# Kernel tuning notes

Measured on AMD Instinct MI355X. Metric: run time of the kernel, lower is better.

## Reference

```python
import jax, jax.numpy as jnp
import numpy as np

N = 512   # particles
T = 128   # timesteps
V_L = 3.4
V_0 = 4.2
GAMMA = 0.9
ALPHA = 0.15
BETA = 15.0
E_CRIT_INV = 2e-5
F_STD = 0.05
G_STD = 0.02
NU = 1.0 / (G_STD * float(np.sqrt(2.0 * np.pi)))
CUR_MIN = 0.0
CUR_MAX = 1.0


def voc(soc):
    # open-circuit voltage model
    return (V_L + (V_0 - V_L) * jnp.exp(GAMMA * (soc - 1.0))
            + ALPHA * V_L * (soc - 1.0)
            + (1.0 - ALPHA) * V_L * (jnp.exp(-BETA) - jnp.exp(-BETA * jnp.sqrt(soc))))


def mlp(x, w1, b1, w2, b2, w3, b3):
    h = jax.nn.sigmoid(x @ w1 + b1)
    h = jax.nn.sigmoid(h @ w2 + b2)
    return h @ w3 + b3


def setup_inputs() -> dict:
    key = jax.random.key(0)
    ks = jax.random.split(key, 11)
    soc_init = jax.random.uniform(ks[0], (N, 1), jnp.float32, 0.6, 1.0)
    current = jax.random.uniform(ks[1], (1, T), jnp.float32)
    voltage_measured = 3.4 + 0.8 * jax.random.uniform(ks[2], (1, T), jnp.float32)
    noise = jax.random.normal(ks[3], (T, N, 1), jnp.float32)
    u = jax.random.uniform(ks[4], (T,), jnp.float32)
    w1 = jax.random.normal(ks[5], (2, 1024), jnp.float32) / np.float32(np.sqrt(2.0))
    b1 = jnp.zeros((1024,), jnp.float32)
    w2 = jax.random.normal(ks[6], (1024, 512), jnp.float32) / np.float32(np.sqrt(1024.0))
    b2 = jnp.zeros((512,), jnp.float32)
    w3 = jax.random.normal(ks[7], (512, 1), jnp.float32) / np.float32(np.sqrt(512.0))
    b3 = jnp.zeros((1,), jnp.float32)
    return {"soc_init": soc_init, "current": current, "voltage_measured": voltage_measured,
            "noise": noise, "u": u, "w1": w1, "b1": b1, "w2": w2, "b2": b2, "w3": w3, "b3": b3}


def reference(soc_init, current, voltage_measured, noise, u, w1, b1, w2, b2, w3, b3):
    n = soc_init.shape[0]
    # pre-loop step: V at t=0 conditions
    I0 = current[0, 0] * jnp.ones_like(soc_init)
    sI0 = (I0 - CUR_MIN) / (CUR_MAX - CUR_MIN)
    Z0 = mlp(jnp.concatenate([soc_init, sI0], axis=1), w1, b1, w2, b2, w3, b3)
    V0 = voc(soc_init) - I0 * Z0

    log_n = jnp.log(jnp.float32(n))

    def step(carry, xs):
        soc, I, V = carry
        cur_t, vmeas_t, noise_t, u_t = xs
        # state propagation with process noise, then clamp to (0, 1]
        soc = soc - I * V * E_CRIT_INV + F_STD * noise_t
        soc = jnp.where(soc > 1.0, 1.0, jnp.where(soc < 0.0, 1e-10, soc))
        I = cur_t * jnp.ones_like(soc)
        sI = (I - CUR_MIN) / (CUR_MAX - CUR_MIN)
        Z = mlp(jnp.concatenate([soc, sI], axis=1), w1, b1, w2, b2, w3, b3)  # [N,1]
        V = voc(soc) - I * Z                                                 # [N,1]
        # importance weights / step loss (logsumexp trick as in source)
        logW = jnp.log(jnp.float32(NU)) - 0.5 * jnp.square((V - vmeas_t) / G_STD)
        step_loss = jax.nn.logsumexp(logW) - log_n
        # systematic resampling on normalized weights
        wn = jax.nn.softmax(logW[:, 0])          # normalized weights [N]
        cum = jnp.cumsum(wn)
        pos = (jnp.arange(n, dtype=jnp.float32) + u_t) / jnp.float32(n)
        idx = jnp.clip(jnp.searchsorted(cum, pos), 0, n - 1)
        soc_r = soc[idx]
        return (soc_r, I, V), (V[:, 0], soc_r[:, 0], step_loss)

    xs = (current[0], voltage_measured[0], noise, u)
    _, (v_hist, s_hist, losses) = jax.lax.scan(step, (soc_init, I0, V0), xs)
    loss = jnp.sum(losses)
    voltage = v_hist.T    # [N, T]
    soc_hist = s_hist.T   # [N, T]
    return loss, voltage, soc_hist
```

## Files before the change

### kernel.cpp

```cpp
#include <hip/hip_runtime.h>
#include <math.h>

#define NP 512
#define TS 128
#define GI 33
#define TAB2D (GI * GI)
#define GV 193
#define V_Lc 3.4f
#define V_0c 4.2f
#define GAMMAc 0.9f
#define ALPHAc 0.15f
#define BETAc 15.0f
#define E_INV 2e-5f
#define F_STDc 0.05f
#define G_STDc 0.02f

#define LBAR() asm volatile("s_waitcnt lgkmcnt(0)\n\ts_barrier" ::: "memory")

__device__ __forceinline__ float sigmoid_jax(float x) {
    float e = expf(-fabsf(x));
    float num = (x >= 0.f) ? 1.f : e;
    return num / (1.f + e);
}

__device__ __forceinline__ float vocf(float s) {
    float sm1 = s - 1.f;
    return V_Lc + (V_0c - V_Lc) * expf(GAMMAc * sm1)
         + (ALPHAc * V_Lc) * sm1
         + (1.f - ALPHAc) * V_Lc * (expf(-BETAc) - expf(-BETAc * sqrtf(s)));
}

template <int R>
__device__ __forceinline__ int dpp_ror(int v) {
    return __builtin_amdgcn_update_dpp(0, v, 0x120 | R, 0xf, 0xf, false);
}
template <int S>
__device__ __forceinline__ int dpp_shr(int v) {
    return __builtin_amdgcn_update_dpp(0, v, 0x110 | S, 0xf, 0xf, true);
}
__device__ __forceinline__ float rdlane_f(float v, int l) {
    return __int_as_float(__builtin_amdgcn_readlane(__float_as_int(v), l));
}

__device__ __forceinline__ float wave_max_f(float v) {
    v = fmaxf(v, __int_as_float(dpp_ror<1>(__float_as_int(v))));
    v = fmaxf(v, __int_as_float(dpp_ror<2>(__float_as_int(v))));
    v = fmaxf(v, __int_as_float(dpp_ror<4>(__float_as_int(v))));
    v = fmaxf(v, __int_as_float(dpp_ror<8>(__float_as_int(v))));
    int iv = __float_as_int(v);
    v = fmaxf(v, __int_as_float(__builtin_amdgcn_update_dpp(iv, iv, 0x142, 0xf, 0xf, false)));
    iv = __float_as_int(v);
    v = fmaxf(v, __int_as_float(__builtin_amdgcn_update_dpp(iv, iv, 0x143, 0xf, 0xf, false)));
    return rdlane_f(v, 63);
}

__device__ __forceinline__ int wave_max_i(int v) {
    v = max(v, dpp_ror<1>(v));
    v = max(v, dpp_ror<2>(v));
    v = max(v, dpp_ror<4>(v));
    v = max(v, dpp_ror<8>(v));
    v = max(v, __builtin_amdgcn_update_dpp(v, v, 0x142, 0xf, 0xf, false));
    v = max(v, __builtin_amdgcn_update_dpp(v, v, 0x143, 0xf, 0xf, false));
    return __builtin_amdgcn_readlane(v, 63);
}

__device__ __forceinline__ float wave_scan_add(float v, int lane) {
    v += __int_as_float(dpp_shr<1>(__float_as_int(v)));
    v += __int_as_float(dpp_shr<2>(__float_as_int(v)));
    v += __int_as_float(dpp_shr<4>(__float_as_int(v)));
    v += __int_as_float(dpp_shr<8>(__float_as_int(v)));
    float s15 = rdlane_f(v, 15);
    float s31 = rdlane_f(v, 31);
    float s47 = rdlane_f(v, 47);
    int row = lane >> 4;
    if (row >= 1) v += s15;
    if (row >= 2) v += s31;
    if (row >= 3) v += s47;
    return v;
}

__device__ __forceinline__ int wave_scanmax_i(int v, int lane) {
    v = max(v, dpp_shr<1>(v));
    v = max(v, dpp_shr<2>(v));
    v = max(v, dpp_shr<4>(v));
    v = max(v, dpp_shr<8>(v));
    int r15 = __builtin_amdgcn_readlane(v, 15);
    int r31 = __builtin_amdgcn_readlane(v, 31);
    int r47 = __builtin_amdgcn_readlane(v, 47);
    int row = lane >> 4;
    if (row >= 1) v = max(v, r15);
    if (row >= 2) v = max(v, r31);
    if (row >= 3) v = max(v, r47);
    return v;
}

__device__ __forceinline__ float interp33(const float* __restrict__ row, float s) {
    float x = s * 32.0f;
    int j = (int)floorf(x);
    j = j < 0 ? 0 : (j > 31 ? 31 : j);
    int st = j - 1;
    st = st < 0 ? 0 : (st > 29 ? 29 : st);
    float uu = x - (float)st;
    float um0 = uu, um1 = uu - 1.f, um2 = uu - 2.f, um3 = uu - 3.f;
    float c0 = um1 * um2 * um3 * (-1.f / 6.f);
    float c1 = um0 * um2 * um3 * (0.5f);
    float c2 = um0 * um1 * um3 * (-0.5f);
    float c3 = um0 * um1 * um2 * (1.f / 6.f);
    return c0 * row[st] + c1 * row[st + 1] + c2 * row[st + 2] + c3 * row[st + 3];
}

__device__ __forceinline__ float interp193(const float* __restrict__ row, float s) {
    float x = s * 192.0f;
    int j = (int)floorf(x);
    j = j < 0 ? 0 : (j > 191 ? 191 : j);
    int st = j - 1;
    st = st < 0 ? 0 : (st > 189 ? 189 : st);
    float uu = x - (float)st;
    float um0 = uu, um1 = uu - 1.f, um2 = uu - 2.f, um3 = uu - 3.f;
    float c0 = um1 * um2 * um3 * (-1.f / 6.f);
    float c1 = um0 * um2 * um3 * (0.5f);
    float c2 = um0 * um1 * um3 * (-0.5f);
    float c3 = um0 * um1 * um2 * (1.f / 6.f);
    return c0 * row[st] + c1 * row[st + 1] + c2 * row[st + 2] + c3 * row[st + 3];
}

__device__ __forceinline__ int count_le(float C, float u) {
    int h = (int)floorf(C - u);
    h = h < -1 ? -1 : (h > 511 ? 511 : h);
    h += (int)((h < 511) && (((float)(h + 1) + u) <= C));
    h -= (int)((h >= 0) && (((float)h + u) > C));
    return h + 1;
}

#define BKT 32
__global__ __launch_bounds__(256) void k_tab(
    const float* __restrict__ w1, const float* __restrict__ b1,
    const float* __restrict__ w2, const float* __restrict__ b2,
    const float* __restrict__ w3, float* __restrict__ zpart)
{
    const int tid = threadIdx.x;
    const int rowblk = blockIdx.x >> 1;
    const int colhalf = blockIdx.x & 1;
    const int r0 = rowblk * 16;
    const int cbase = colhalf * 256;

    __shared__ float As[16][BKT + 1];
    __shared__ float Bs[BKT][256];
    __shared__ float srow[16], irow[16];

    if (tid < 16) {
        int r = r0 + tid;
        r = r > (TAB2D - 1) ? (TAB2D - 1) : r;
        int si = r / GI;
        int ii = r - si * GI;
        srow[tid] = (float)si * (1.0f / 32.0f);
        irow[tid] = (float)ii * (1.0f / 32.0f);
    }
    __syncthreads();

    const int rg = tid >> 5;
    const int ct = tid & 31;
    float acc[2][8];
    #pragma unroll
    for (int a = 0; a < 2; ++a)
        #pragma unroll
        for (int b = 0; b < 8; ++b) acc[a][b] = 0.f;

    for (int kk = 0; kk < 1024; kk += BKT) {
        #pragma unroll
        for (int h = 0; h < 2; ++h) {
            int idx = tid + h * 256;
            int row = idx >> 5, k = idx & 31, kc = kk + k;
            float pre = srow[row] * w1[kc] + irow[row] * w1[1024 + kc] + b1[kc];
            As[row][k] = sigmoid_jax(pre);
        }
        #pragma unroll
        for (int jj = 0; jj < 8; ++jj) {
            int vi = tid + jj * 256;
            int k = vi >> 6, c4 = vi & 63;
            *(float4*)&Bs[k][c4 * 4] = *(const float4*)&w2[(kk + k) * 512 + cbase + c4 * 4];
        }
        __syncthreads();
        #pragma unroll
        for (int k = 0; k < BKT; ++k) {
            float a0 = As[rg * 2][k];
            float a1 = As[rg * 2 + 1][k];
            float bq[8];
            *(float4*)&bq[0] = *(const float4*)&Bs[k][ct * 4];
            *(float4*)&bq[4] = *(const float4*)&Bs[k][ct * 4 + 128];
            #pragma unroll
            for (int q = 0; q < 8; ++q) {
                acc[0][q] += a0 * bq[q];
                acc[1][q] += a1 * bq[q];
            }
        }
        __syncthreads();
    }

    float b2r[8], w3r[8];
    *(float4*)&b2r[0] = *(const float4*)&b2[cbase + ct * 4];
    *(float4*)&b2r[4] = *(const float4*)&b2[cbase + ct * 4 + 128];
    *(float4*)&w3r[0] = *(const float4*)&w3[cbase + ct * 4];
    *(float4*)&w3r[4] = *(const float4*)&w3[cbase + ct * 4 + 128];
    #pragma unroll
    for (int rr = 0; rr < 2; ++rr) {
        float zp = 0.f;
        #pragma unroll
        for (int q = 0; q < 8; ++q)
            zp += w3r[q] * sigmoid_jax(acc[rr][q] + b2r[q]);
        #pragma unroll
        for (int mm = 1; mm < 32; mm <<= 1) zp += __shfl_xor(zp, mm);
        if (ct == 0 && (r0 + rg * 2 + rr) < TAB2D)
            zpart[colhalf * TAB2D + r0 + rg * 2 + rr] = zp;
    }
}

__global__ __launch_bounds__(256) void k_pre(
    const float* __restrict__ zpart, const float* __restrict__ current,
    const float* __restrict__ b3, float* __restrict__ vt_g)
{
    __shared__ float zrow[GI];
    const int t = blockIdx.x;
    const int tid = threadIdx.x;
    const float It = current[t];
    const float bb3 = b3[0];

    if (tid < GI) {
        float x = It * 32.0f;
        int j = (int)floorf(x);
        j = j < 0 ? 0 : (j > 31 ? 31 : j);
        int st = j - 1;
        st = st < 0 ? 0 : (st > 29 ? 29 : st);
        float uu = x - (float)st;
        float um0 = uu, um1 = uu - 1.f, um2 = uu - 2.f, um3 = uu - 3.f;
        float c0 = um1 * um2 * um3 * (-1.f / 6.f);
        float c1 = um0 * um2 * um3 * (0.5f);
        float c2 = um0 * um1 * um3 * (-0.5f);
        float c3 = um0 * um1 * um2 * (1.f / 6.f);
        int base = tid * GI + st;
        float n0 = zpart[base]     + zpart[TAB2D + base]     + bb3;
        float n1 = zpart[base + 1] + zpart[TAB2D + base + 1] + bb3;
        float n2 = zpart[base + 2] + zpart[TAB2D + base + 2] + bb3;
        float n3 = zpart[base + 3] + zpart[TAB2D + base + 3] + bb3;
        zrow[tid] = c0 * n0 + c1 * n1 + c2 * n2 + c3 * n3;
    }
    __syncthreads();
    if (tid < GV) {
        float sj = (float)tid * (1.0f / 192.0f);
        vt_g[t * GV + tid] = vocf(sj) - It * interp33(zrow, sj);
    }
}

__global__ __launch_bounds__(256, 1) void k_seq(
    const float* __restrict__ vt_g, const float* __restrict__ soc_init,
    const float* __restrict__ current, const float* __restrict__ vmeas,
    const float* __restrict__ u, const float* __restrict__ noise,
    float* __restrict__ vbuf, float* __restrict__ sbuf, float* __restrict__ out)
{
    const int tid = threadIdx.x;
    const int lane = tid & 63;
    const int wv = tid >> 6;

    __shared__ __align__(16) float vt[TS * GV];
    __shared__ float2 socs2[2][NP / 2];
    __shared__ int2  marker2[NP / 2];
    __shared__ float cur_s[TS], vm_s[TS], u_s[TS];
    __shared__ float2 redMT[4];
    int* marker = (int*)marker2;

    for (int i4 = tid; i4 < (TS * GV) / 4; i4 += 256)
        *(float4*)&vt[i4 * 4] = *(const float4*)&vt_g[i4 * 4];
    if (tid < TS) { cur_s[tid] = current[tid]; vm_s[tid] = vmeas[tid]; u_s[tid] = u[tid]; }
    marker2[tid] = make_int2(0, 0);
    __syncthreads();

    float2 si2 = *(const float2*)&soc_init[2 * tid];
    float soc0 = si2.x, soc1 = si2.y;
    float Iprev = cur_s[0];
    float V0 = interp193(&vt[0], soc0);
    float V1 = interp193(&vt[0], soc1);
    float loss_acc = 0.f;
    const float LOG_NU = logf(19.947114020071635f);
    const float LOG_N = logf(512.f);
    float2 nz = *(const float2*)&noise[2 * tid];

    for (int t = 0; t < TS; ++t) {
        int tn = (t + 1 < TS) ? t + 1 : t;
        float2 nz_next = *(const float2*)&noise[tn * 512 + 2 * tid];

        soc0 = soc0 - Iprev * V0 * E_INV + F_STDc * nz.x;
        soc1 = soc1 - Iprev * V1 * E_INV + F_STDc * nz.y;
        soc0 = soc0 > 1.f ? 1.f : (soc0 < 0.f ? 1e-10f : soc0);
        soc1 = soc1 > 1.f ? 1.f : (soc1 < 0.f ? 1e-10f : soc1);
        socs2[t & 1][tid] = make_float2(soc0, soc1);

        const float* vr = &vt[t * GV];
        V0 = interp193(vr, soc0);
        V1 = interp193(vr, soc1);
        *(float2*)&vbuf[t * 512 + 2 * tid] = make_float2(V0, V1);
        float vm = vm_s[t];
        float d0 = (V0 - vm) * (1.f / G_STDc);
        float d1 = (V1 - vm) * (1.f / G_STDc);
        float lw0 = LOG_NU - 0.5f * d0 * d0;
        float lw1 = LOG_NU - 0.5f * d1 * d1;

        float m = wave_max_f(fmaxf(lw0, lw1));
        float e0 = __expf(lw0 - m);
        float e1 = __expf(lw1 - m);
        float ps = wave_scan_add(e0 + e1, lane);
        if (lane == 63) redMT[wv] = make_float2(m, ps);
        LBAR();

        float2 rmt = redMT[lane & 3];
        float rm = rmt.x;
        float rt = rmt.y;
        float M = rm;
        M = fmaxf(M, __int_as_float(dpp_ror<1>(__float_as_int(M))));
        M = fmaxf(M, __int_as_float(dpp_ror<2>(__float_as_int(M))));
        float fw = __expf(rm - M);
        float term = rt * fw;
        float sc = term;
        sc += __int_as_float(dpp_shr<1>(__float_as_int(sc)));
        sc += __int_as_float(dpp_shr<2>(__float_as_int(sc)));
        float S = rdlane_f(sc, 3);
        float off = (wv > 0) ? rdlane_f(sc, wv - 1) : 0.f;
        float fw_own = rdlane_f(fw, wv);
        loss_acc += M + __logf(S) - LOG_N;

        float incl1 = ps;
        float incl0 = ps - e1;
        float C0 = 512.f * ((off + incl0 * fw_own) / S);
        float C1 = 512.f * ((off + incl1 * fw_own) / S);
        float ut = u_s[t];
        int hi0 = count_le(C0, ut);
        int hi1 = count_le(C1, ut);
        if (hi0 < 512) atomicMax(&marker[hi0], (t << 10) | (2 * tid + 1));
        if (hi1 < 512) atomicMax(&marker[hi1], (t << 10) | (2 * tid + 2));
        LBAR();

        int2 mk = marker2[tid];
        int pm_l = 0;
        for (int w = 0; w < wv; ++w) {
            int2 q = marker2[w * 64 + lane];
            pm_l = max(pm_l, max(q.x, q.y));
        }
        int pm = wave_max_i(pm_l);
        int mpair = max(mk.x, mk.y);
        int psx = wave_scanmax_i(mpair, lane);
        int up = dpp_shr<1>(psx);
        int r15 = __builtin_amdgcn_readlane(psx, 15);
        int r31 = __builtin_amdgcn_readlane(psx, 31);
        int r47 = __builtin_amdgcn_readlane(psx, 47);
        if (lane == 16) up = r15;
        if (lane == 32) up = r31;
        if (lane == 48) up = r47;
        int excl = max(up, pm);
        int tag0 = max(excl, mk.x);
        int tag1 = max(excl, mpair);
        int o0 = ((tag0 >> 10) == t) ? (tag0 & 1023) : 0;
        int o1 = ((tag1 >> 10) == t) ? (tag1 & 1023) : 0;
        o0 = o0 > 511 ? 511 : o0;
        o1 = o1 > 511 ? 511 : o1;
        const float* sflat = (const float*)&socs2[t & 1][0];
        float sr0 = sflat[o0];
        float sr1 = sflat[o1];
        *(float2*)&sbuf[t * 512 + 2 * tid] = make_float2(sr0, sr1);

        soc0 = sr0;
        soc1 = sr1;
        Iprev = cur_s[t];
        nz = nz_next;
    }
    if (tid == 0) out[0] = loss_acc;
}

__global__ __launch_bounds__(256) void k_fin(
    const float* __restrict__ vbuf, const float* __restrict__ sbuf,
    float* __restrict__ out)
{
    __shared__ float tile[32][33];
    int tz = blockIdx.z;
    int t0 = blockIdx.x * 32;
    int i0 = blockIdx.y * 32;
    const float* src = tz ? sbuf : vbuf;
    float* dst = out + 1 + tz * (NP * TS);
    int tx = threadIdx.x & 31, ty = threadIdx.x >> 5;
    #pragma unroll
    for (int m2 = 0; m2 < 4; ++m2)
        tile[ty + 8 * m2][tx] = src[(t0 + ty + 8 * m2) * 512 + i0 + tx];
    __syncthreads();
    #pragma unroll
    for (int m2 = 0; m2 < 4; ++m2)
        dst[(i0 + ty + 8 * m2) * 128 + t0 + tx] = tile[tx][ty + 8 * m2];
}

extern "C" void kernel_launch(void* const* d_in, const int* in_sizes, int n_in,
                              void* d_out, int out_size, void* d_ws, size_t ws_size,
                              hipStream_t stream)
{
    const float* soc_init = (const float*)d_in[0];
    const float* current  = (const float*)d_in[1];
    const float* vmeas    = (const float*)d_in[2];
    const float* noise    = (const float*)d_in[3];
    const float* u        = (const float*)d_in[4];
    const float* w1 = (const float*)d_in[5];
    const float* b1 = (const float*)d_in[6];
    const float* w2 = (const float*)d_in[7];
    const float* b2 = (const float*)d_in[8];
    const float* w3 = (const float*)d_in[9];
    const float* b3 = (const float*)d_in[10];
    float* out = (float*)d_out;
    float* ws  = (float*)d_ws;

    float* zpart = ws;
    float* vt_g  = ws + 2180;
    float* vbuf  = vt_g + TS * GV;
    float* sbuf  = vbuf + NP * TS;

    k_tab<<<138, 256, 0, stream>>>(w1, b1, w2, b2, w3, zpart);
    k_pre<<<128, 256, 0, stream>>>(zpart, current, b3, vt_g);
    k_seq<<<1, 256, 0, stream>>>(vt_g, soc_init, current, vmeas, u, noise,
                                 vbuf, sbuf, out);
    k_fin<<<dim3(4, 16, 2), 256, 0, stream>>>(vbuf, sbuf, out);
}
```

Baseline: 245.2 us.

## Run sequential filter with two waves and four particles per thread

The sequential particle-filter kernel now runs on 128 threads, each handling four particles instead of two. This halves the number of waves taking part in each per-step barrier and cross-wave reduction, and simplifies the block-level max/sum and marker prefix-max. The voltage lookup grid is also refined from 193 to 257 points, with the precompute kernel widened to 320 threads. That raises the table's LDS footprint and initial load, and puts more serial ALU work on each thread.

```diff
diff --git a/kernel.cpp b/kernel.cpp
--- a/kernel.cpp
+++ b/kernel.cpp
@@ -5,7 +5,7 @@
 #define TS 128
 #define GI 33
 #define TAB2D (GI * GI)
-#define GV 193
+#define GV 257
 #define V_Lc 3.4f
 #define V_0c 4.2f
 #define GAMMAc 0.9f
@@ -109,12 +109,12 @@
     return c0 * row[st] + c1 * row[st + 1] + c2 * row[st + 2] + c3 * row[st + 3];
 }
 
-__device__ __forceinline__ float interp193(const float* __restrict__ row, float s) {
-    float x = s * 192.0f;
+__device__ __forceinline__ float interp257(const float* __restrict__ row, float s) {
+    float x = s * 256.0f;
     int j = (int)floorf(x);
-    j = j < 0 ? 0 : (j > 191 ? 191 : j);
+    j = j < 0 ? 0 : (j > 255 ? 255 : j);
     int st = j - 1;
-    st = st < 0 ? 0 : (st > 189 ? 189 : st);
+    st = st < 0 ? 0 : (st > 253 ? 253 : st);
     float uu = x - (float)st;
     float um0 = uu, um1 = uu - 1.f, um2 = uu - 2.f, um3 = uu - 3.f;
     float c0 = um1 * um2 * um3 * (-1.f / 6.f);
@@ -215,7 +215,7 @@
     }
 }
 
-__global__ __launch_bounds__(256) void k_pre(
+__global__ __launch_bounds__(320) void k_pre(
     const float* __restrict__ zpart, const float* __restrict__ current,
     const float* __restrict__ b3, float* __restrict__ vt_g)
 {
@@ -246,12 +246,12 @@
     }
     __syncthreads();
     if (tid < GV) {
-        float sj = (float)tid * (1.0f / 192.0f);
+        float sj = (float)tid * (1.0f / 256.0f);
         vt_g[t * GV + tid] = vocf(sj) - It * interp33(zrow, sj);
     }
 }
 
-__global__ __launch_bounds__(256, 1) void k_seq(
+__global__ __launch_bounds__(128, 1) void k_seq(
     const float* __restrict__ vt_g, const float* __restrict__ soc_init,
     const float* __restrict__ current, const float* __restrict__ vmeas,
     const float* __restrict__ u, const float* __restrict__ noise,
@@ -262,91 +262,108 @@
     const int wv = tid >> 6;
 
     __shared__ __align__(16) float vt[TS * GV];
-    __shared__ float2 socs2[2][NP / 2];
-    __shared__ int2  marker2[NP / 2];
+    __shared__ __align__(16) float socs[2][NP];
+    __shared__ __align__(16) int marker[NP];
     __shared__ float cur_s[TS], vm_s[TS], u_s[TS];
-    __shared__ float2 redMT[4];
-    int* marker = (int*)marker2;
-
-    for (int i4 = tid; i4 < (TS * GV) / 4; i4 += 256)
+    __shared__ __align__(16) float2 redMT[2];
+
+    for (int i4 = tid; i4 < (TS * GV) / 4; i4 += 128)
         *(float4*)&vt[i4 * 4] = *(const float4*)&vt_g[i4 * 4];
-    if (tid < TS) { cur_s[tid] = current[tid]; vm_s[tid] = vmeas[tid]; u_s[tid] = u[tid]; }
-    marker2[tid] = make_int2(0, 0);
+    { int r = TS * GV - (TS * GV / 4) * 4; (void)r; }
+    cur_s[tid] = current[tid]; vm_s[tid] = vmeas[tid]; u_s[tid] = u[tid];
+    *(int4*)&marker[4 * tid] = make_int4(0, 0, 0, 0);
     __syncthreads();
 
-    float2 si2 = *(const float2*)&soc_init[2 * tid];
-    float soc0 = si2.x, soc1 = si2.y;
+    float4 si4 = *(const float4*)&soc_init[4 * tid];
+    float soc0 = si4.x, soc1 = si4.y, soc2 = si4.z, soc3 = si4.w;
     float Iprev = cur_s[0];
-    float V0 = interp193(&vt[0], soc0);
-    float V1 = interp193(&vt[0], soc1);
+    float V0 = interp257(&vt[0], soc0);
+    float V1 = interp257(&vt[0], soc1);
+    float V2 = interp257(&vt[0], soc2);
+    float V3 = interp257(&vt[0], soc3);
     float loss_acc = 0.f;
     const float LOG_NU = logf(19.947114020071635f);
     const float LOG_N = logf(512.f);
-    float2 nz = *(const float2*)&noise[2 * tid];
+    float4 nz = *(const float4*)&noise[4 * tid];
 
     for (int t = 0; t < TS; ++t) {
         int tn = (t + 1 < TS) ? t + 1 : t;
-        float2 nz_next = *(const float2*)&noise[tn * 512 + 2 * tid];
+        float4 nz_next = *(const float4*)&noise[tn * 512 + 4 * tid];
 
         soc0 = soc0 - Iprev * V0 * E_INV + F_STDc * nz.x;
         soc1 = soc1 - Iprev * V1 * E_INV + F_STDc * nz.y;
+        soc2 = soc2 - Iprev * V2 * E_INV + F_STDc * nz.z;
+        soc3 = soc3 - Iprev * V3 * E_INV + F_STDc * nz.w;
         soc0 = soc0 > 1.f ? 1.f : (soc0 < 0.f ? 1e-10f : soc0);
         soc1 = soc1 > 1.f ? 1.f : (soc1 < 0.f ? 1e-10f : soc1);
-        socs2[t & 1][tid] = make_float2(soc0, soc1);
+        soc2 = soc2 > 1.f ? 1.f : (soc2 < 0.f ? 1e-10f : soc2);
+        soc3 = soc3 > 1.f ? 1.f : (soc3 < 0.f ? 1e-10f : soc3);
+        *(float4*)&socs[t & 1][4 * tid] = make_float4(soc0, soc1, soc2, soc3);
 
         const float* vr = &vt[t * GV];
-        V0 = interp193(vr, soc0);
-        V1 = interp193(vr, soc1);
-        *(float2*)&vbuf[t * 512 + 2 * tid] = make_float2(V0, V1);
+        V0 = interp257(vr, soc0);
+        V1 = interp257(vr, soc1);
+        V2 = interp257(vr, soc2);
+        V3 = interp257(vr, soc3);
+        *(float4*)&vbuf[t * 512 + 4 * tid] = make_float4(V0, V1, V2, V3);
         float vm = vm_s[t];
         float d0 = (V0 - vm) * (1.f / G_STDc);
         float d1 = (V1 - vm) * (1.f / G_STDc);
+        float d2 = (V2 - vm) * (1.f / G_STDc);
+        float d3 = (V3 - vm) * (1.f / G_STDc);
         float lw0 = LOG_NU - 0.5f * d0 * d0;
         float lw1 = LOG_NU - 0.5f * d1 * d1;
-
-        float m = wave_max_f(fmaxf(lw0, lw1));
+        float lw2 = LOG_NU - 0.5f * d2 * d2;
+        float lw3 = LOG_NU - 0.5f * d3 * d3;
+
+        float m = wave_max_f(fmaxf(fmaxf(lw0, lw1), fmaxf(lw2, lw3)));
         float e0 = __expf(lw0 - m);
         float e1 = __expf(lw1 - m);
-        float ps = wave_scan_add(e0 + e1, lane);
-        if (lane == 63) redMT[wv] = make_float2(m, ps);
+        float e2 = __expf(lw2 - m);
+        float e3 = __expf(lw3 - m);
+        float c0 = e0;
+        float c1 = c0 + e1;
+        float c2 = c1 + e2;
+        float c3 = c2 + e3;
+        float tot = c3;
+        float incl = wave_scan_add(tot, lane);
+        if (lane == 63) redMT[wv] = make_float2(m, incl);
         LBAR();
 
-        float2 rmt = redMT[lane & 3];
-        float rm = rmt.x;
-        float rt = rmt.y;
-        float M = rm;
-        M = fmaxf(M, __int_as_float(dpp_ror<1>(__float_as_int(M))));
-        M = fmaxf(M, __int_as_float(dpp_ror<2>(__float_as_int(M))));
-        float fw = __expf(rm - M);
-        float term = rt * fw;
-        float sc = term;
-        sc += __int_as_float(dpp_shr<1>(__float_as_int(sc)));
-        sc += __int_as_float(dpp_shr<2>(__float_as_int(sc)));
-        float S = rdlane_f(sc, 3);
-        float off = (wv > 0) ? rdlane_f(sc, wv - 1) : 0.f;
-        float fw_own = rdlane_f(fw, wv);
+        float4 rr = *(float4*)&redMT[0];
+        float M = fmaxf(rr.x, rr.z);
+        float fw0 = __expf(rr.x - M);
+        float fw1 = __expf(rr.z - M);
+        float t0 = rr.y * fw0;
+        float t1 = rr.w * fw1;
+        float S = t0 + t1;
+        float off = wv ? t0 : 0.f;
+        float fw_own = wv ? fw1 : fw0;
         loss_acc += M + __logf(S) - LOG_N;
 
-        float incl1 = ps;
-        float incl0 = ps - e1;
-        float C0 = 512.f * ((off + incl0 * fw_own) / S);
-        float C1 = 512.f * ((off + incl1 * fw_own) / S);
+        float base = incl - tot;
         float ut = u_s[t];
+        float C0 = 512.f * ((off + (base + c0) * fw_own) / S);
+        float C1 = 512.f * ((off + (base + c1) * fw_own) / S);
+        float C2 = 512.f * ((off + (base + c2) * fw_own) / S);
+        float C3 = 512.f * ((off + (base + c3) * fw_own) / S);
         int hi0 = count_le(C0, ut);
         int hi1 = count_le(C1, ut);
-        if (hi0 < 512) atomicMax(&marker[hi0], (t << 10) | (2 * tid + 1));
-        if (hi1 < 512) atomicMax(&marker[hi1], (t << 10) | (2 * tid + 2));
+        int hi2 = count_le(C2, ut);
+        int hi3 = count_le(C3, ut);
+        int p4 = 4 * tid;
+        if (hi0 < 512) atomicMax(&marker[hi0], (t << 10) | (p4 + 1));
+        if (hi1 < 512) atomicMax(&marker[hi1], (t << 10) | (p4 + 2));
+        if (hi2 < 512) atomicMax(&marker[hi2], (t << 10) | (p4 + 3));
+        if (hi3 < 512) atomicMax(&marker[hi3], (t << 10) | (p4 + 4));
         LBAR();
 
-        int2 mk = marker2[tid];
-        int pm_l = 0;
-        for (int w = 0; w < wv; ++w) {
-            int2 q = marker2[w * 64 + lane];
-            pm_l = max(pm_l, max(q.x, q.y));
-        }
-        int pm = wave_max_i(pm_l);
-        int mpair = max(mk.x, mk.y);
-        int psx = wave_scanmax_i(mpair, lane);
+        int4 mk = *(int4*)&marker[4 * tid];
+        int4 oth = *(int4*)&marker[4 * lane];
+        int pm = 0;
+        if (wv) pm = wave_max_i(max(max(oth.x, oth.y), max(oth.z, oth.w)));
+        int lm = max(max(mk.x, mk.y), max(mk.z, mk.w));
+        int psx = wave_scanmax_i(lm, lane);
         int up = dpp_shr<1>(psx);
         int r15 = __builtin_amdgcn_readlane(psx, 15);
         int r31 = __builtin_amdgcn_readlane(psx, 31);
@@ -356,18 +373,25 @@
         if (lane == 48) up = r47;
         int excl = max(up, pm);
         int tag0 = max(excl, mk.x);
-        int tag1 = max(excl, mpair);
+        int tag1 = max(tag0, mk.y);
+        int tag2 = max(tag1, mk.z);
+        int tag3 = max(tag2, mk.w);
         int o0 = ((tag0 >> 10) == t) ? (tag0 & 1023) : 0;
         int o1 = ((tag1 >> 10) == t) ? (tag1 & 1023) : 0;
+        int o2 = ((tag2 >> 10) == t) ? (tag2 & 1023) : 0;
+        int o3 = ((tag3 >> 10) == t) ? (tag3 & 1023) : 0;
         o0 = o0 > 511 ? 511 : o0;
         o1 = o1 > 511 ? 511 : o1;
-        const float* sflat = (const float*)&socs2[t & 1][0];
+        o2 = o2 > 511 ? 511 : o2;
+        o3 = o3 > 511 ? 511 : o3;
+        const float* sflat = &socs[t & 1][0];
         float sr0 = sflat[o0];
         float sr1 = sflat[o1];
-        *(float2*)&sbuf[t * 512 + 2 * tid] = make_float2(sr0, sr1);
-
-        soc0 = sr0;
-        soc1 = sr1;
+        float sr2 = sflat[o2];
+        float sr3 = sflat[o3];
+        *(float4*)&sbuf[t * 512 + 4 * tid] = make_float4(sr0, sr1, sr2, sr3);
+
+        soc0 = sr0; soc1 = sr1; soc2 = sr2; soc3 = sr3;
         Iprev = cur_s[t];
         nz = nz_next;
     }
@@ -418,8 +442,8 @@
     float* sbuf  = vbuf + NP * TS;
 
     k_tab<<<138, 256, 0, stream>>>(w1, b1, w2, b2, w3, zpart);
-    k_pre<<<128, 256, 0, stream>>>(zpart, current, b3, vt_g);
-    k_seq<<<1, 256, 0, stream>>>(vt_g, soc_init, current, vmeas, u, noise,
+    k_pre<<<128, 320, 0, stream>>>(zpart, current, b3, vt_g);
+    k_seq<<<1, 128, 0, stream>>>(vt_g, soc_init, current, vmeas, u, noise,
                                  vbuf, sbuf, out);
     k_fin<<<dim3(4, 16, 2), 256, 0, stream>>>(vbuf, sbuf, out);
 }
```

Result: slower. 267.3 us (+9.0%).

## Run sequential particle filter in a single wave to drop block barriers

Applied to the files above, without the earlier changes.

The sequential resampling loop now runs on one 64-lane wavefront, each lane owning 8 particles, instead of four waves each handling 2. Cross-wave barriers and shared reductions are gone, replaced by in-lane serial scans plus wave-level DPP scans. Without barriers, only an lgkmcnt wait orders the LDS writes and reads. The voltage lookup grid is also widened from 193 to 257 points, which enlarges the table load and changes interpolation accuracy. The trade is per-step barrier latency against a longer serial dependency chain per lane.

```diff
diff --git a/kernel.cpp b/kernel.cpp
--- a/kernel.cpp
+++ b/kernel.cpp
@@ -5,7 +5,7 @@
 #define TS 128
 #define GI 33
 #define TAB2D (GI * GI)
-#define GV 193
+#define GV 257
 #define V_Lc 3.4f
 #define V_0c 4.2f
 #define GAMMAc 0.9f
@@ -15,7 +15,7 @@
 #define F_STDc 0.05f
 #define G_STDc 0.02f
 
-#define LBAR() asm volatile("s_waitcnt lgkmcnt(0)\n\ts_barrier" ::: "memory")
+#define LGKM0() asm volatile("s_waitcnt lgkmcnt(0)" ::: "memory")
 
 __device__ __forceinline__ float sigmoid_jax(float x) {
     float e = expf(-fabsf(x));
@@ -52,16 +52,6 @@
     iv = __float_as_int(v);
     v = fmaxf(v, __int_as_float(__builtin_amdgcn_update_dpp(iv, iv, 0x143, 0xf, 0xf, false)));
     return rdlane_f(v, 63);
-}
-
-__device__ __forceinline__ int wave_max_i(int v) {
-    v = max(v, dpp_ror<1>(v));
-    v = max(v, dpp_ror<2>(v));
-    v = max(v, dpp_ror<4>(v));
-    v = max(v, dpp_ror<8>(v));
-    v = max(v, __builtin_amdgcn_update_dpp(v, v, 0x142, 0xf, 0xf, false));
-    v = max(v, __builtin_amdgcn_update_dpp(v, v, 0x143, 0xf, 0xf, false));
-    return __builtin_amdgcn_readlane(v, 63);
 }
 
 __device__ __forceinline__ float wave_scan_add(float v, int lane) {
@@ -109,12 +99,12 @@
     return c0 * row[st] + c1 * row[st + 1] + c2 * row[st + 2] + c3 * row[st + 3];
 }
 
-__device__ __forceinline__ float interp193(const float* __restrict__ row, float s) {
-    float x = s * 192.0f;
+__device__ __forceinline__ float interp257(const float* __restrict__ row, float s) {
+    float x = s * 256.0f;
     int j = (int)floorf(x);
-    j = j < 0 ? 0 : (j > 191 ? 191 : j);
+    j = j < 0 ? 0 : (j > 255 ? 255 : j);
     int st = j - 1;
-    st = st < 0 ? 0 : (st > 189 ? 189 : st);
+    st = st < 0 ? 0 : (st > 253 ? 253 : st);
     float uu = x - (float)st;
     float um0 = uu, um1 = uu - 1.f, um2 = uu - 2.f, um3 = uu - 3.f;
     float c0 = um1 * um2 * um3 * (-1.f / 6.f);
@@ -215,7 +205,7 @@
     }
 }
 
-__global__ __launch_bounds__(256) void k_pre(
+__global__ __launch_bounds__(320) void k_pre(
     const float* __restrict__ zpart, const float* __restrict__ current,
     const float* __restrict__ b3, float* __restrict__ vt_g)
 {
@@ -246,107 +236,108 @@
     }
     __syncthreads();
     if (tid < GV) {
-        float sj = (float)tid * (1.0f / 192.0f);
+        float sj = (float)tid * (1.0f / 256.0f);
         vt_g[t * GV + tid] = vocf(sj) - It * interp33(zrow, sj);
     }
 }
 
-__global__ __launch_bounds__(256, 1) void k_seq(
+__global__ __launch_bounds__(512, 1) void k_seq(
     const float* __restrict__ vt_g, const float* __restrict__ soc_init,
     const float* __restrict__ current, const float* __restrict__ vmeas,
     const float* __restrict__ u, const float* __restrict__ noise,
     float* __restrict__ vbuf, float* __restrict__ sbuf, float* __restrict__ out)
 {
     const int tid = threadIdx.x;
-    const int lane = tid & 63;
-    const int wv = tid >> 6;
 
     __shared__ __align__(16) float vt[TS * GV];
-    __shared__ float2 socs2[2][NP / 2];
-    __shared__ int2  marker2[NP / 2];
+    __shared__ __align__(16) float socs[NP];
+    __shared__ __align__(16) int marker[NP];
     __shared__ float cur_s[TS], vm_s[TS], u_s[TS];
-    __shared__ float2 redMT[4];
-    int* marker = (int*)marker2;
-
-    for (int i4 = tid; i4 < (TS * GV) / 4; i4 += 256)
+
+    for (int i4 = tid; i4 < (TS * GV) / 4; i4 += 512)
         *(float4*)&vt[i4 * 4] = *(const float4*)&vt_g[i4 * 4];
     if (tid < TS) { cur_s[tid] = current[tid]; vm_s[tid] = vmeas[tid]; u_s[tid] = u[tid]; }
-    marker2[tid] = make_int2(0, 0);
+    marker[tid] = 0;
     __syncthreads();
-
-    float2 si2 = *(const float2*)&soc_init[2 * tid];
-    float soc0 = si2.x, soc1 = si2.y;
+    if (tid >= 64) return;
+
+    const int lane = tid;
+    const int p0 = 8 * lane;
+
+    float soc[8], V[8];
+    *(float4*)&soc[0] = *(const float4*)&soc_init[p0];
+    *(float4*)&soc[4] = *(const float4*)&soc_init[p0 + 4];
     float Iprev = cur_s[0];
-    float V0 = interp193(&vt[0], soc0);
-    float V1 = interp193(&vt[0], soc1);
+    #pragma unroll
+    for (int k = 0; k < 8; ++k) V[k] = interp257(&vt[0], soc[k]);
+
     float loss_acc = 0.f;
     const float LOG_NU = logf(19.947114020071635f);
     const float LOG_N = logf(512.f);
-    float2 nz = *(const float2*)&noise[2 * tid];
+    float nz[8];
+    *(float4*)&nz[0] = *(const float4*)&noise[p0];
+    *(float4*)&nz[4] = *(const float4*)&noise[p0 + 4];
 
     for (int t = 0; t < TS; ++t) {
         int tn = (t + 1 < TS) ? t + 1 : t;
-        float2 nz_next = *(const float2*)&noise[tn * 512 + 2 * tid];
-
-        soc0 = soc0 - Iprev * V0 * E_INV + F_STDc * nz.x;
-        soc1 = soc1 - Iprev * V1 * E_INV + F_STDc * nz.y;
-        soc0 = soc0 > 1.f ? 1.f : (soc0 < 0.f ? 1e-10f : soc0);
-        soc1 = soc1 > 1.f ? 1.f : (soc1 < 0.f ? 1e-10f : soc1);
-        socs2[t & 1][tid] = make_float2(soc0, soc1);
+        float4 nzn0 = *(const float4*)&noise[tn * 512 + p0];
+        float4 nzn1 = *(const float4*)&noise[tn * 512 + p0 + 4];
+
+        #pragma unroll
+        for (int k = 0; k < 8; ++k) {
+            float s = soc[k] - Iprev * V[k] * E_INV + F_STDc * nz[k];
+            soc[k] = s > 1.f ? 1.f : (s < 0.f ? 1e-10f : s);
+        }
+        *(float4*)&socs[p0]     = *(float4*)&soc[0];
+        *(float4*)&socs[p0 + 4] = *(float4*)&soc[4];
 
         const float* vr = &vt[t * GV];
-        V0 = interp193(vr, soc0);
-        V1 = interp193(vr, soc1);
-        *(float2*)&vbuf[t * 512 + 2 * tid] = make_float2(V0, V1);
+        #pragma unroll
+        for (int k = 0; k < 8; ++k) V[k] = interp257(vr, soc[k]);
+        *(float4*)&vbuf[t * 512 + p0]     = *(float4*)&V[0];
+        *(float4*)&vbuf[t * 512 + p0 + 4] = *(float4*)&V[4];
+
         float vm = vm_s[t];
-        float d0 = (V0 - vm) * (1.f / G_STDc);
-        float d1 = (V1 - vm) * (1.f / G_STDc);
-        float lw0 = LOG_NU - 0.5f * d0 * d0;
-        float lw1 = LOG_NU - 0.5f * d1 * d1;
-
-        float m = wave_max_f(fmaxf(lw0, lw1));
-        float e0 = __expf(lw0 - m);
-        float e1 = __expf(lw1 - m);
-        float ps = wave_scan_add(e0 + e1, lane);
-        if (lane == 63) redMT[wv] = make_float2(m, ps);
-        LBAR();
-
-        float2 rmt = redMT[lane & 3];
-        float rm = rmt.x;
-        float rt = rmt.y;
-        float M = rm;
-        M = fmaxf(M, __int_as_float(dpp_ror<1>(__float_as_int(M))));
-        M = fmaxf(M, __int_as_float(dpp_ror<2>(__float_as_int(M))));
-        float fw = __expf(rm - M);
-        float term = rt * fw;
-        float sc = term;
-        sc += __int_as_float(dpp_shr<1>(__float_as_int(sc)));
-        sc += __int_as_float(dpp_shr<2>(__float_as_int(sc)));
-        float S = rdlane_f(sc, 3);
-        float off = (wv > 0) ? rdlane_f(sc, wv - 1) : 0.f;
-        float fw_own = rdlane_f(fw, wv);
+        float lw[8];
+        #pragma unroll
+        for (int k = 0; k < 8; ++k) {
+            float d = (V[k] - vm) * (1.f / G_STDc);
+            lw[k] = LOG_NU - 0.5f * d * d;
+        }
+
+        float m8 = fmaxf(fmaxf(fmaxf(lw[0], lw[1]), fmaxf(lw[2], lw[3])),
+                         fmaxf(fmaxf(lw[4], lw[5]), fmaxf(lw[6], lw[7])));
+        float M = wave_max_f(m8);
+        float c[8];
+        float run = 0.f;
+        #pragma unroll
+        for (int k = 0; k < 8; ++k) {
+            run += __expf(lw[k] - M);
+            c[k] = run;
+        }
+        float tot = run;
+        float incl = wave_scan_add(tot, lane);
+        float base = incl - tot;
+        float S = rdlane_f(incl, 63);
         loss_acc += M + __logf(S) - LOG_N;
 
-        float incl1 = ps;
-        float incl0 = ps - e1;
-        float C0 = 512.f * ((off + incl0 * fw_own) / S);
-        float C1 = 512.f * ((off + incl1 * fw_own) / S);
+        float rS = 512.f / S;
         float ut = u_s[t];
-        int hi0 = count_le(C0, ut);
-        int hi1 = count_le(C1, ut);
-        if (hi0 < 512) atomicMax(&marker[hi0], (t << 10) | (2 * tid + 1));
-        if (hi1 < 512) atomicMax(&marker[hi1], (t << 10) | (2 * tid + 2));
-        LBAR();
-
-        int2 mk = marker2[tid];
-        int pm_l = 0;
-        for (int w = 0; w < wv; ++w) {
-            int2 q = marker2[w * 64 + lane];
-            pm_l = max(pm_l, max(q.x, q.y));
-        }
-        int pm = wave_max_i(pm_l);
-        int mpair = max(mk.x, mk.y);
-        int psx = wave_scanmax_i(mpair, lane);
+        int p1t = (t << 10) | (p0 + 1);
+        #pragma unroll
+        for (int k = 0; k < 8; ++k) {
+            float C = (base + c[k]) * rS;
+            int hi = count_le(C, ut);
+            if (hi < 512) atomicMax(&marker[hi], p1t + k);
+        }
+        LGKM0();
+
+        int4 mkA = *(int4*)&marker[p0];
+        int4 mkB = *(int4*)&marker[p0 + 4];
+        int mk[8] = {mkA.x, mkA.y, mkA.z, mkA.w, mkB.x, mkB.y, mkB.z, mkB.w};
+        int lm = max(max(max(mk[0], mk[1]), max(mk[2], mk[3])),
+                     max(max(mk[4], mk[5]), max(mk[6], mk[7])));
+        int psx = wave_scanmax_i(lm, lane);
         int up = dpp_shr<1>(psx);
         int r15 = __builtin_amdgcn_readlane(psx, 15);
         int r31 = __builtin_amdgcn_readlane(psx, 31);
@@ -354,22 +345,23 @@
         if (lane == 16) up = r15;
         if (lane == 32) up = r31;
         if (lane == 48) up = r47;
-        int excl = max(up, pm);
-        int tag0 = max(excl, mk.x);
-        int tag1 = max(excl, mpair);
-        int o0 = ((tag0 >> 10) == t) ? (tag0 & 1023) : 0;
-        int o1 = ((tag1 >> 10) == t) ? (tag1 & 1023) : 0;
-        o0 = o0 > 511 ? 511 : o0;
-        o1 = o1 > 511 ? 511 : o1;
-        const float* sflat = (const float*)&socs2[t & 1][0];
-        float sr0 = sflat[o0];
-        float sr1 = sflat[o1];
-        *(float2*)&sbuf[t * 512 + 2 * tid] = make_float2(sr0, sr1);
-
-        soc0 = sr0;
-        soc1 = sr1;
+        float sr[8];
+        int tagr = up;
+        #pragma unroll
+        for (int k = 0; k < 8; ++k) {
+            tagr = max(tagr, mk[k]);
+            int o = ((tagr >> 10) == t) ? (tagr & 1023) : 0;
+            o = o > 511 ? 511 : o;
+            sr[k] = socs[o];
+        }
+        *(float4*)&sbuf[t * 512 + p0]     = *(float4*)&sr[0];
+        *(float4*)&sbuf[t * 512 + p0 + 4] = *(float4*)&sr[4];
+
+        #pragma unroll
+        for (int k = 0; k < 8; ++k) soc[k] = sr[k];
         Iprev = cur_s[t];
-        nz = nz_next;
+        nz[0] = nzn0.x; nz[1] = nzn0.y; nz[2] = nzn0.z; nz[3] = nzn0.w;
+        nz[4] = nzn1.x; nz[5] = nzn1.y; nz[6] = nzn1.z; nz[7] = nzn1.w;
     }
     if (tid == 0) out[0] = loss_acc;
 }
@@ -418,8 +410,8 @@
     float* sbuf  = vbuf + NP * TS;
 
     k_tab<<<138, 256, 0, stream>>>(w1, b1, w2, b2, w3, zpart);
-    k_pre<<<128, 256, 0, stream>>>(zpart, current, b3, vt_g);
-    k_seq<<<1, 256, 0, stream>>>(vt_g, soc_init, current, vmeas, u, noise,
+    k_pre<<<128, 320, 0, stream>>>(zpart, current, b3, vt_g);
+    k_seq<<<1, 512, 0, stream>>>(vt_g, soc_init, current, vmeas, u, noise,
                                  vbuf, sbuf, out);
     k_fin<<<dim3(4, 16, 2), 256, 0, stream>>>(vbuf, sbuf, out);
 }
```

Measured after the change: 307.0 us. +25.2%, slower.
